# Kernel optimization log

Hardware: AMD Instinct MI355X
Metric: run time of the kernel (lower is better)

## Reference

```python
import jax, jax.numpy as jnp
import numpy as np

N = 50000        # nodes
E = 800000       # edges
IN, H1, H2 = 512, 256, 128
NEG_SLOPE = 0.2


def setup_inputs() -> dict:
    key = jax.random.key(0)
    k = jax.random.split(key, 6)
    X = jax.random.normal(k[0], (N, IN), jnp.float32)
    edge_index = jax.random.randint(k[1], (2, E), 0, N, dtype=jnp.int64)
    # GCNConv params: linear weight (no bias in lin) + additive bias
    W1 = jax.random.normal(k[2], (IN, H1), jnp.float32) / np.sqrt(IN).astype(np.float32)
    b1 = jnp.zeros((H1,), jnp.float32)
    W2 = jax.random.normal(k[3], (H1, H2), jnp.float32) / np.sqrt(H1).astype(np.float32)
    b2 = jnp.zeros((H2,), jnp.float32)
    return {"X": X, "edge_index": edge_index, "W1": W1, "b1": b1, "W2": W2, "b2": b2}


def gcn_conv(x, edge_index, W, b):
    """PyG GCNConv: X' = D^{-1/2} (A + I) D^{-1/2} (X W) + b."""
    src, dst = edge_index[0], edge_index[1]
    # degree with self-loops (unit edge weights)
    deg = jnp.zeros((N,), x.dtype).at[dst].add(jnp.asarray(1.0, x.dtype)) + 1.0
    dinv = jax.lax.rsqrt(deg)
    h = x @ W                                   # dense transform first (in >= out)
    coef = dinv[src] * dinv[dst]                # [E]
    msgs = h[src] * coef[:, None]               # [E, out]
    agg = jax.ops.segment_sum(msgs, dst, num_segments=N)
    agg = agg + (dinv * dinv)[:, None] * h      # self-loop contribution
    return agg + b


def reference(X, edge_index, W1, b1, W2, b2):
    Z = jax.nn.leaky_relu(gcn_conv(X, edge_index, W1, b1), NEG_SLOPE)
    Z = jax.nn.leaky_relu(gcn_conv(Z, edge_index, W2, b2), NEG_SLOPE)
    return Z
```

## Files before the change

kernel.cpp:

```cpp
#include <hip/hip_runtime.h>

constexpr int N_NODES = 50000;
constexpr int N_EDGES = 800000;
constexpr int F_IN  = 512;
constexpr int F_H1  = 256;
constexpr int F_H2  = 128;

typedef short  short8  __attribute__((ext_vector_type(8)));
typedef float  f32x4   __attribute__((ext_vector_type(4)));
typedef unsigned short us4 __attribute__((ext_vector_type(4)));

__device__ __forceinline__ unsigned short bf16_rn(float f) {
  unsigned int u = __float_as_uint(f);
  return (unsigned short)((u + 0x7FFFu + ((u >> 16) & 1u)) >> 16);
}
__device__ __forceinline__ float bf16_tof(unsigned short h) {
  return __uint_as_float(((unsigned int)h) << 16);
}


__global__ __launch_bounds__(256) void k_count(const int* __restrict__ dst,
                                               int* __restrict__ cnt, int e) {
  int i = blockIdx.x * 256 + threadIdx.x;
  if (i < e) atomicAdd(&cnt[dst[i]], 1);
}

__global__ __launch_bounds__(1024) void k_scan(const int* __restrict__ cnt,
                                               int* __restrict__ rowstart,
                                               int* __restrict__ cursor,
                                               float* __restrict__ dinv, int n) {
  __shared__ int wsum[16];
  __shared__ int carry_s;
  const int t = threadIdx.x;
  const int wid = t >> 6, lane = t & 63;
  if (t == 0) { carry_s = 0; rowstart[0] = 0; }
  __syncthreads();
  for (int base = 0; base < n; base += 4096) {
    const int i0 = base + t * 4;
    int v[4];
    if (i0 + 4 <= n) {
      const int4 v4 = *(const int4*)&cnt[i0];
      v[0] = v4.x; v[1] = v4.y; v[2] = v4.z; v[3] = v4.w;
    } else {
#pragma unroll
      for (int j = 0; j < 4; ++j) v[j] = (i0 + j < n) ? cnt[i0 + j] : 0;
    }
#pragma unroll
    for (int j = 0; j < 4; ++j)
      if (i0 + j < n) dinv[i0 + j] = rsqrtf((float)v[j] + 1.0f);
    const int tsum = v[0] + v[1] + v[2] + v[3];
    int x = tsum;
#pragma unroll
    for (int off = 1; off < 64; off <<= 1) {
      int y = __shfl_up(x, off);
      if (lane >= off) x += y;
    }
    if (lane == 63) wsum[wid] = x;
    __syncthreads();
    if (wid == 0) {
      int s = (lane < 16) ? wsum[lane] : 0;
#pragma unroll
      for (int off = 1; off < 16; off <<= 1) {
        int y = __shfl_up(s, off);
        if (lane >= off) s += y;
      }
      if (lane < 16) wsum[lane] = s;
    }
    __syncthreads();
    const int carry = carry_s;
    const int woff = (wid == 0) ? 0 : wsum[wid - 1];
    int run = carry + woff + x - tsum;
#pragma unroll
    for (int j = 0; j < 4; ++j) {
      if (i0 + j < n) {
        cursor[i0 + j] = run;
        run += v[j];
        rowstart[i0 + j + 1] = run;
      }
    }
    __syncthreads();
    if (t == 1023) carry_s = carry + woff + x;
    __syncthreads();
  }
}

__global__ __launch_bounds__(256) void k_fill(const int* __restrict__ src,
                                              const int* __restrict__ dst,
                                              int* __restrict__ cursor,
                                              const float* __restrict__ dinv,
                                              int2* __restrict__ csr, int e) {
  int i = blockIdx.x * 256 + threadIdx.x;
  if (i < e) {
    const int s = src[i], d = dst[i];
    int slot = atomicAdd(&cursor[d], 1);
    csr[slot] = make_int2(s, __float_as_int(dinv[s] * dinv[d]));
  }
}

__global__ __launch_bounds__(256) void k_wsplit2(const float* __restrict__ W1,
                                                 unsigned short* __restrict__ W1h,
                                                 unsigned short* __restrict__ W1l,
                                                 const float* __restrict__ W2,
                                                 unsigned short* __restrict__ W2h,
                                                 unsigned short* __restrict__ W2l) {
  constexpr int T1 = F_IN * F_H1;
  constexpr int T2 = F_H1 * F_H2;
  int id = blockIdx.x * 256 + threadIdx.x;
  if (id < T1) {
    int n = id / F_IN, k = id - n * F_IN;
    float f = W1[(size_t)k * F_H1 + n];
    unsigned short h = bf16_rn(f);
    W1h[id] = h;
    W1l[id] = bf16_rn(f - bf16_tof(h));
  } else if (id < T1 + T2) {
    int id2 = id - T1;
    int n = id2 / F_H1, k = id2 - n * F_H1;
    float f = W2[(size_t)k * F_H2 + n];
    unsigned short h = bf16_rn(f);
    W2h[id2] = h;
    W2l[id2] = bf16_rn(f - bf16_tof(h));
  }
}

template <bool A_IS_F32>
__global__ __launch_bounds__(256) void k_mm(const float* __restrict__ Af,
                                            const unsigned short* __restrict__ Ah,
                                            const unsigned short* __restrict__ Al,
                                            const unsigned short* __restrict__ Bth,
                                            const unsigned short* __restrict__ Btl,
                                            float* __restrict__ C,
                                            unsigned short* __restrict__ Cb,
                                            int M, int N, int K) {
  __shared__ unsigned short Ah_s[128 * 64];
  __shared__ unsigned short Al_s[128 * 64];
  __shared__ unsigned short Bh_s[128 * 64];
  __shared__ unsigned short Bl_s[128 * 64];
  const int tid = threadIdx.x;
  const int wid = tid >> 6, lane = tid & 63;
  const int wm = wid >> 1, wn = wid & 1;
  const int lr = lane & 15, lg = lane >> 4;
  const int row0 = blockIdx.x * 128, col0 = blockIdx.y * 128;

  f32x4 acc[4][4] = {};

  for (int k0 = 0; k0 < K; k0 += 64) {
#pragma unroll
    for (int c = 0; c < 4; ++c) {
      const int i8 = c * 256 + tid;
      const int r = i8 >> 3, g = i8 & 7;
      const int gr = row0 + r;
      const int gs = g ^ (r & 7);
      if (A_IS_F32) {
        float4 f0 = make_float4(0.f, 0.f, 0.f, 0.f), f1 = f0;
        if (gr < M) {
          const float* ap = Af + (size_t)gr * K + k0 + g * 8;
          f0 = *(const float4*)ap;
          f1 = *(const float4*)(ap + 4);
        }
        const float fv[8] = {f0.x, f0.y, f0.z, f0.w, f1.x, f1.y, f1.z, f1.w};
        unsigned short hv[8], lv[8];
#pragma unroll
        for (int j = 0; j < 8; ++j) {
          hv[j] = bf16_rn(fv[j]);
          lv[j] = bf16_rn(fv[j] - bf16_tof(hv[j]));
        }
        us4* dh = (us4*)&Ah_s[r * 64 + gs * 8];
        us4* dl = (us4*)&Al_s[r * 64 + gs * 8];
        dh[0] = us4{hv[0], hv[1], hv[2], hv[3]};
        dh[1] = us4{hv[4], hv[5], hv[6], hv[7]};
        dl[0] = us4{lv[0], lv[1], lv[2], lv[3]};
        dl[1] = us4{lv[4], lv[5], lv[6], lv[7]};
      } else {
        short8 h8 = {}, l8 = {};
        if (gr < M) {
          h8 = *(const short8*)&Ah[(size_t)gr * K + k0 + g * 8];
          l8 = *(const short8*)&Al[(size_t)gr * K + k0 + g * 8];
        }
        *(short8*)&Ah_s[r * 64 + gs * 8] = h8;
        *(short8*)&Al_s[r * 64 + gs * 8] = l8;
      }
    }
#pragma unroll
    for (int c = 0; c < 4; ++c) {
      const int i8 = c * 256 + tid;
      const int r = i8 >> 3, g = i8 & 7;
      const int gcol = col0 + r;
      const int gs = g ^ (r & 7);
      *(short8*)&Bh_s[r * 64 + gs * 8] =
          *(const short8*)&Bth[(size_t)gcol * K + k0 + g * 8];
      *(short8*)&Bl_s[r * 64 + gs * 8] =
          *(const short8*)&Btl[(size_t)gcol * K + k0 + g * 8];
    }
    __syncthreads();
#pragma unroll
    for (int kk = 0; kk < 2; ++kk) {
      short8 ah[4], al[4], bh[4], bl[4];
#pragma unroll
      for (int m = 0; m < 4; ++m) {
        const int r = wm * 64 + m * 16 + lr;
        const int g = kk * 4 + lg;
        const int off = r * 64 + (g ^ (r & 7)) * 8;
        ah[m] = *(const short8*)&Ah_s[off];
        al[m] = *(const short8*)&Al_s[off];
      }
#pragma unroll
      for (int n = 0; n < 4; ++n) {
        const int r = wn * 64 + n * 16 + lr;
        const int g = kk * 4 + lg;
        const int off = r * 64 + (g ^ (r & 7)) * 8;
        bh[n] = *(const short8*)&Bh_s[off];
        bl[n] = *(const short8*)&Bl_s[off];
      }
#pragma unroll
      for (int m = 0; m < 4; ++m)
#pragma unroll
        for (int n = 0; n < 4; ++n)
          acc[m][n] = __builtin_amdgcn_mfma_f32_16x16x32_bf16(ah[m], bh[n],
                                                              acc[m][n], 0, 0, 0);
#pragma unroll
      for (int m = 0; m < 4; ++m)
#pragma unroll
        for (int n = 0; n < 4; ++n) {
          acc[m][n] = __builtin_amdgcn_mfma_f32_16x16x32_bf16(ah[m], bl[n],
                                                              acc[m][n], 0, 0, 0);
          acc[m][n] = __builtin_amdgcn_mfma_f32_16x16x32_bf16(al[m], bh[n],
                                                              acc[m][n], 0, 0, 0);
        }
    }
    __syncthreads();
  }
#pragma unroll
  for (int m = 0; m < 4; ++m) {
#pragma unroll
    for (int j = 0; j < 4; ++j) {
      const int row = row0 + wm * 64 + m * 16 + (lane >> 4) * 4 + j;
      if (row < M) {
        const size_t boff = (size_t)row * N + col0 + wn * 64 + (lane & 15);
        float* cp = C + boff;
#pragma unroll
        for (int n = 0; n < 4; ++n) cp[n * 16] = acc[m][n][j];
        if (Cb) {
          unsigned short* cbp = Cb + boff;
#pragma unroll
          for (int n = 0; n < 4; ++n) cbp[n * 16] = bf16_rn(acc[m][n][j]);
        }
      }
    }
  }
}

template <int F, bool SPLIT_OUT, bool BF16G>
__global__ __launch_bounds__(256) void k_agg(const float* __restrict__ hf,
                                             const unsigned short* __restrict__ hb,
                                             const int* __restrict__ rowstart,
                                             const int2* __restrict__ csr,
                                             const float* __restrict__ dinv,
                                             const float* __restrict__ bias,
                                             float* __restrict__ outp,
                                             unsigned short* __restrict__ outh,
                                             unsigned short* __restrict__ outl,
                                             int n) {
  constexpr int V = F / 64;
  const int node = (blockIdx.x * 256 + threadIdx.x) >> 6;
  const int lane = threadIdx.x & 63;
  if (node >= n) return;
  const float dn = dinv[node];
  const int e0 = rowstart[node];
  const int cnt = rowstart[node + 1] - e0;
  const int2* cp = csr + e0;
  float acc[V] = {};
  int i = 0;

  auto gather = [&](int s, float f[V]) {
    if constexpr (BF16G) {
      if constexpr (V == 4) {
        const uint2 u = *(const uint2*)(hb + (size_t)s * F + lane * 4);
        f[0] = __uint_as_float(u.x << 16);
        f[1] = __uint_as_float(u.x & 0xffff0000u);
        f[2] = __uint_as_float(u.y << 16);
        f[3] = __uint_as_float(u.y & 0xffff0000u);
      } else {
        const unsigned int u = *(const unsigned int*)(hb + (size_t)s * F + lane * 2);
        f[0] = __uint_as_float(u << 16);
        f[1] = __uint_as_float(u & 0xffff0000u);
      }
    } else {
      if constexpr (V == 4) {
        const float4 v = *(const float4*)(hf + (size_t)s * F + lane * 4);
        f[0] = v.x; f[1] = v.y; f[2] = v.z; f[3] = v.w;
      } else {
        const float2 v = *(const float2*)(hf + (size_t)s * F + lane * 2);
        f[0] = v.x; f[1] = v.y;
      }
    }
  };

  for (; i + 4 <= cnt; i += 4) {
    const int2 p0 = cp[i], p1 = cp[i + 1], p2 = cp[i + 2], p3 = cp[i + 3];
    float f0[V], f1[V], f2[V], f3[V];
    gather(p0.x, f0);
    gather(p1.x, f1);
    gather(p2.x, f2);
    gather(p3.x, f3);
    const float c0 = __int_as_float(p0.y), c1 = __int_as_float(p1.y);
    const float c2 = __int_as_float(p2.y), c3 = __int_as_float(p3.y);
#pragma unroll
    for (int j = 0; j < V; ++j)
      acc[j] += c0 * f0[j] + c1 * f1[j] + c2 * f2[j] + c3 * f3[j];
  }
  for (; i < cnt; ++i) {
    const int2 p = cp[i];
    const float c = __int_as_float(p.y);
    float f[V];
    gather(p.x, f);
#pragma unroll
    for (int j = 0; j < V; ++j) acc[j] += c * f[j];
  }

  const float sc = dn * dn;
  const float* hp = hf + (size_t)node * F + lane * V;
  const float* bp = bias + lane * V;
  float r[V];
#pragma unroll
  for (int j = 0; j < V; ++j) {
    float t = acc[j] + sc * hp[j] + bp[j];
    r[j] = fmaxf(t, 0.2f * t);
  }
  if constexpr (SPLIT_OUT) {
    unsigned short hh[V], ll[V];
#pragma unroll
    for (int j = 0; j < V; ++j) {
      hh[j] = bf16_rn(r[j]);
      ll[j] = bf16_rn(r[j] - bf16_tof(hh[j]));
    }
    if constexpr (V == 4) {
      *(us4*)&outh[(size_t)node * F + lane * 4] = us4{hh[0], hh[1], hh[2], hh[3]};
      *(us4*)&outl[(size_t)node * F + lane * 4] = us4{ll[0], ll[1], ll[2], ll[3]};
    } else {
#pragma unroll
      for (int j = 0; j < V; ++j) {
        outh[(size_t)node * F + lane * V + j] = hh[j];
        outl[(size_t)node * F + lane * V + j] = ll[j];
      }
    }
  } else {
    float* op = outp + (size_t)node * F + lane * V;
    if constexpr (V == 4) {
      *(float4*)op = make_float4(r[0], r[1], r[2], r[3]);
    } else {
      *(float2*)op = make_float2(r[0], r[1]);
    }
  }
}

extern "C" void kernel_launch(void* const* d_in, const int* in_sizes, int n_in,
                              void* d_out, int out_size, void* d_ws, size_t ws_size,
                              hipStream_t stream) {
  const float* X  = (const float*)d_in[0];
  const int*   ei = (const int*)d_in[1];
  const float* W1 = (const float*)d_in[2];
  const float* b1 = (const float*)d_in[3];
  const float* W2 = (const float*)d_in[4];
  const float* b2 = (const float*)d_in[5];
  float* out = (float*)d_out;
  const int* src = ei;
  const int* dst = ei + N_EDGES;

  char* p0 = (char*)d_ws;
  char* p = p0;
  float* h1 = (float*)p;                    p += (size_t)N_NODES * F_H1 * 4;
  unsigned short* z1h = (unsigned short*)p; p += (size_t)N_NODES * F_H1 * 2;
  unsigned short* z1l = (unsigned short*)p; p += (size_t)N_NODES * F_H1 * 2;
  unsigned short* Wt1h = (unsigned short*)p; p += (size_t)F_IN * F_H1 * 2;
  unsigned short* Wt1l = (unsigned short*)p; p += (size_t)F_IN * F_H1 * 2;
  unsigned short* Wt2h = (unsigned short*)p; p += (size_t)F_H1 * F_H2 * 2;
  unsigned short* Wt2l = (unsigned short*)p; p += (size_t)F_H1 * F_H2 * 2;
  float* dinv = (float*)p;                  p += 50048 * 4;
  int* counts = (int*)p;                    p += 50048 * 4;
  int* rowstart = (int*)p;                  p += 50056 * 4;
  int* cursor = (int*)p;                    p += 50048 * 4;
  int2* csr = (int2*)p;                     p += (size_t)N_EDGES * 8;
  unsigned short* h1b = (unsigned short*)p; p += (size_t)N_NODES * F_H1 * 2;
  unsigned short* h2b = h1b;
  float* h2 = h1;
  const bool GB = (size_t)(p - p0) <= ws_size;

  hipMemsetAsync(counts, 0, N_NODES * sizeof(int), stream);
  k_count<<<(N_EDGES + 255) / 256, 256, 0, stream>>>(dst, counts, N_EDGES);
  k_scan<<<1, 1024, 0, stream>>>(counts, rowstart, cursor, dinv, N_NODES);
  k_fill<<<(N_EDGES + 255) / 256, 256, 0, stream>>>(src, dst, cursor, dinv, csr,
                                                    N_EDGES);

  k_wsplit2<<<(F_IN * F_H1 + F_H1 * F_H2 + 255) / 256, 256, 0, stream>>>(
      W1, Wt1h, Wt1l, W2, Wt2h, Wt2l);

  dim3 g1((N_NODES + 127) / 128, F_H1 / 128);
  k_mm<true><<<g1, 256, 0, stream>>>(X, nullptr, nullptr, Wt1h, Wt1l, h1,
                                     GB ? h1b : nullptr, N_NODES, F_H1, F_IN);
  if (GB)
    k_agg<F_H1, true, true><<<(N_NODES + 3) / 4, 256, 0, stream>>>(
        h1, h1b, rowstart, csr, dinv, b1, nullptr, z1h, z1l, N_NODES);
  else
    k_agg<F_H1, true, false><<<(N_NODES + 3) / 4, 256, 0, stream>>>(
        h1, nullptr, rowstart, csr, dinv, b1, nullptr, z1h, z1l, N_NODES);

  dim3 g2((N_NODES + 127) / 128, F_H2 / 128);
  k_mm<false><<<g2, 256, 0, stream>>>(nullptr, z1h, z1l, Wt2h, Wt2l, h2,
                                      GB ? h2b : nullptr, N_NODES, F_H2, F_H1);
  if (GB)
    k_agg<F_H2, false, true><<<(N_NODES + 3) / 4, 256, 0, stream>>>(
        h2, h2b, rowstart, csr, dinv, b2, out, nullptr, nullptr, N_NODES);
  else
    k_agg<F_H2, false, false><<<(N_NODES + 3) / 4, 256, 0, stream>>>(
        h2, nullptr, rowstart, csr, dinv, b2, out, nullptr, nullptr, N_NODES);
}
```

Measured before the change: 352.2 us.

## Prefetch next GEMM K-tile into registers while computing current tile

Restructures the split-bf16 GEMM main loop so global loads for the next K-tile are issued into registers before the MFMA work on the current tile, then written to shared memory at the top of the next iteration. This aims to hide global memory latency behind compute. It raises register pressure (prefetch buffers for A and B), which may reduce occupancy or cause spills, especially in the fp32-A variant.

```diff
diff --git a/kernel.cpp b/kernel.cpp
--- a/kernel.cpp
+++ b/kernel.cpp
@@ -143,55 +143,76 @@
 
   f32x4 acc[4][4] = {};
 
-  for (int k0 = 0; k0 < K; k0 += 64) {
+  float4 af0[4], af1[4];
+  short8 ahr[4], alr[4];
+  short8 bhr[4], blr[4];
+
+  const int r_ld = tid >> 3, g_ld = tid & 7;
+  const bool arow_ok = (row0 + r_ld) < M;
+
+  auto load_tile = [&](int k0) {
 #pragma unroll
     for (int c = 0; c < 4; ++c) {
-      const int i8 = c * 256 + tid;
-      const int r = i8 >> 3, g = i8 & 7;
+      const int r = c * 32 + r_ld;
       const int gr = row0 + r;
-      const int gs = g ^ (r & 7);
       if (A_IS_F32) {
-        float4 f0 = make_float4(0.f, 0.f, 0.f, 0.f), f1 = f0;
+        af0[c] = make_float4(0.f, 0.f, 0.f, 0.f);
+        af1[c] = af0[c];
         if (gr < M) {
-          const float* ap = Af + (size_t)gr * K + k0 + g * 8;
-          f0 = *(const float4*)ap;
-          f1 = *(const float4*)(ap + 4);
+          const float* ap = Af + (size_t)gr * K + k0 + g_ld * 8;
+          af0[c] = *(const float4*)ap;
+          af1[c] = *(const float4*)(ap + 4);
         }
-        const float fv[8] = {f0.x, f0.y, f0.z, f0.w, f1.x, f1.y, f1.z, f1.w};
+      } else {
+        ahr[c] = short8{};
+        alr[c] = short8{};
+        if (gr < M) {
+          ahr[c] = *(const short8*)&Ah[(size_t)gr * K + k0 + g_ld * 8];
+          alr[c] = *(const short8*)&Al[(size_t)gr * K + k0 + g_ld * 8];
+        }
+      }
+      const int gcol = col0 + r;
+      bhr[c] = *(const short8*)&Bth[(size_t)gcol * K + k0 + g_ld * 8];
+      blr[c] = *(const short8*)&Btl[(size_t)gcol * K + k0 + g_ld * 8];
+    }
+  };
+
+  auto store_tile = [&]() {
+#pragma unroll
+    for (int c = 0; c < 4; ++c) {
+      const int r = c * 32 + r_ld;
+      const int gs = g_ld ^ (r & 7);
+      const int doff = r * 64 + gs * 8;
+      if (A_IS_F32) {
+        const float fv[8] = {af0[c].x, af0[c].y, af0[c].z, af0[c].w,
+                             af1[c].x, af1[c].y, af1[c].z, af1[c].w};
         unsigned short hv[8], lv[8];
 #pragma unroll
         for (int j = 0; j < 8; ++j) {
           hv[j] = bf16_rn(fv[j]);
           lv[j] = bf16_rn(fv[j] - bf16_tof(hv[j]));
         }
-        us4* dh = (us4*)&Ah_s[r * 64 + gs * 8];
-        us4* dl = (us4*)&Al_s[r * 64 + gs * 8];
+        us4* dh = (us4*)&Ah_s[doff];
+        us4* dl = (us4*)&Al_s[doff];
         dh[0] = us4{hv[0], hv[1], hv[2], hv[3]};
         dh[1] = us4{hv[4], hv[5], hv[6], hv[7]};
         dl[0] = us4{lv[0], lv[1], lv[2], lv[3]};
         dl[1] = us4{lv[4], lv[5], lv[6], lv[7]};
       } else {
-        short8 h8 = {}, l8 = {};
-        if (gr < M) {
-          h8 = *(const short8*)&Ah[(size_t)gr * K + k0 + g * 8];
-          l8 = *(const short8*)&Al[(size_t)gr * K + k0 + g * 8];
-        }
-        *(short8*)&Ah_s[r * 64 + gs * 8] = h8;
-        *(short8*)&Al_s[r * 64 + gs * 8] = l8;
-      }
-    }
-#pragma unroll
-    for (int c = 0; c < 4; ++c) {
-      const int i8 = c * 256 + tid;
-      const int r = i8 >> 3, g = i8 & 7;
-      const int gcol = col0 + r;
-      const int gs = g ^ (r & 7);
-      *(short8*)&Bh_s[r * 64 + gs * 8] =
-          *(const short8*)&Bth[(size_t)gcol * K + k0 + g * 8];
-      *(short8*)&Bl_s[r * 64 + gs * 8] =
-          *(const short8*)&Btl[(size_t)gcol * K + k0 + g * 8];
-    }
-    __syncthreads();
+        *(short8*)&Ah_s[doff] = ahr[c];
+        *(short8*)&Al_s[doff] = alr[c];
+      }
+      *(short8*)&Bh_s[doff] = bhr[c];
+      *(short8*)&Bl_s[doff] = blr[c];
+    }
+  };
+
+  const int nsteps = K >> 6;
+  load_tile(0);
+  for (int s = 0; s < nsteps; ++s) {
+    store_tile();
+    __syncthreads();
+    if (s + 1 < nsteps) load_tile((s + 1) << 6);
 #pragma unroll
     for (int kk = 0; kk < 2; ++kk) {
       short8 ah[4], al[4], bh[4], bl[4];
```

New measurement: 348.8 us. No clear change (-1.0%).
